# Optimization experiments

Measured on AMD Instinct MI355X. Metric: run time of the kernel, lower is better.

The kernel has to match this reference:

```python
import jax, jax.numpy as jnp
import numpy as np

NUM_LAYERS = 4
D_MODEL = 2
N_HALF = 32  # d_state // 2 complex modes
B, L = 512, 10000


def setup_inputs() -> dict:
    key = jax.random.key(0)
    ks = jax.random.split(key, 10)
    x = jax.random.normal(ks[0], (B, L, 3), dtype=jnp.float32)
    W1 = jax.random.normal(ks[1], (2, 3), dtype=jnp.float32) / np.float32(np.sqrt(3.0))
    b1 = jax.random.normal(ks[2], (2,), dtype=jnp.float32) * 0.1
    W2 = jax.random.normal(ks[3], (2, 2), dtype=jnp.float32) / np.float32(np.sqrt(2.0))
    b2 = jax.random.normal(ks[4], (2,), dtype=jnp.float32) * 0.1
    # S4D kernel params (stacked over layers)
    dt_min, dt_max = 1e-3, 1e-1
    log_dt = (jax.random.uniform(ks[5], (NUM_LAYERS, D_MODEL), dtype=jnp.float32)
              * np.float32(np.log(dt_max) - np.log(dt_min)) + np.float32(np.log(dt_min)))
    log_A_real = jnp.log(0.5 * jnp.ones((NUM_LAYERS, D_MODEL, N_HALF), dtype=jnp.float32))
    A_imag = (np.float32(np.pi) * jnp.arange(N_HALF, dtype=jnp.float32)
              * jnp.ones((NUM_LAYERS, D_MODEL, 1), dtype=jnp.float32))
    C = jax.random.normal(ks[6], (NUM_LAYERS, D_MODEL, N_HALF, 2), dtype=jnp.float32) * np.float32(0.5 ** 0.5)
    D = jax.random.normal(ks[7], (NUM_LAYERS, D_MODEL), dtype=jnp.float32)
    Wout = jax.random.normal(ks[8], (NUM_LAYERS, 2 * D_MODEL, D_MODEL), dtype=jnp.float32) / np.float32(np.sqrt(D_MODEL))
    bout = jax.random.normal(ks[9], (NUM_LAYERS, 2 * D_MODEL), dtype=jnp.float32) * 0.1
    return dict(x=x, W1=W1, b1=b1, W2=W2, b2=b2, log_dt=log_dt,
                log_A_real=log_A_real, A_imag=A_imag, C=C, D=D, Wout=Wout, bout=bout)


def _s4d_kernel(log_dt, log_A_real, A_imag, C, Lk):
    # log_dt: (H,), log_A_real/A_imag: (H,N), C: (H,N,2) -> kernel (H,Lk)
    dt = jnp.exp(log_dt)                              # (H,)
    Cc = C[..., 0] + 1j * C[..., 1]                   # (H,N) complex
    A = -jnp.exp(log_A_real) + 1j * A_imag            # (H,N)
    dtA = A * dt[:, None]                             # (H,N)
    K = dtA[:, :, None] * jnp.arange(Lk)              # (H,N,Lk)
    Cn = Cc * (jnp.exp(dtA) - 1.0) / A                # (H,N)
    return 2.0 * jnp.einsum('hn,hnl->hl', Cn, jnp.exp(K)).real


def reference(x, W1, b1, W2, b2, log_dt, log_A_real, A_imag, C, D, Wout, bout):
    Lseq = x.shape[1]
    h = x @ W1.T + b1                                 # (B,L,2)
    u = jnp.transpose(h, (0, 2, 1))                   # (B,H,L)
    for i in range(NUM_LAYERS):
        k = _s4d_kernel(log_dt[i], log_A_real[i], A_imag[i], C[i], Lseq)  # (H,L)
        kf = jnp.fft.rfft(k, n=2 * Lseq)              # (H,L+1)
        uf = jnp.fft.rfft(u, n=2 * Lseq)              # (B,H,L+1)
        y = jnp.fft.irfft(uf * kf, n=2 * Lseq)[..., :Lseq]  # linear conv via 2L FFT
        y = y + u * D[i][:, None]                     # skip connection
        y = jax.nn.gelu(y, approximate=False)
        y = jnp.einsum('oh,bhl->bol', Wout[i], y) + bout[i][None, :, None]  # Conv1d(H,2H,1)
        a, g = jnp.split(y, 2, axis=1)                # GLU over channel dim
        u = a * jax.nn.sigmoid(g)
    h = jnp.transpose(u, (0, 2, 1))                   # (B,L,2)
    return h @ W2.T + b2
```

## Files before the change

### kernel.cpp

```cpp
#include <hip/hip_runtime.h>
#include <hip/hip_bf16.h>
#include <math.h>

#define BB 512
#define LL 10000
#define HH 2
#define NN 32
#define NL 4
#define TT 64
#define CHK 157
#define CPAD 160
#define BL (BB*LL)

#define OFF_U0   0
#define OFF_U1   10240000
#define OFF_S0   20480000
#define OFF_S1   30769152
#define OFF_TAB  41058304

typedef _Float16 half8 __attribute__((ext_vector_type(8)));
typedef float f32x4 __attribute__((ext_vector_type(4)));

__global__ void setup_kernel(const float* __restrict__ log_dt,
                             const float* __restrict__ log_A_real,
                             const float* __restrict__ A_imag,
                             const float* __restrict__ Cin,
                             float* __restrict__ lam, float* __restrict__ lamT,
                             float* __restrict__ Cn, float* __restrict__ Kt,
                             float* __restrict__ P) {
    int ih = blockIdx.x;
    int tid = threadIdx.x;
    __shared__ float s_dtA[NN * 2];
    __shared__ float s_Cn[NN * 2];
    float dt = expf(log_dt[ih]);
    if (tid < NN) {
        int n = tid;
        float aRe = -expf(log_A_real[ih * NN + n]);
        float aIm = A_imag[ih * NN + n];
        float dRe = aRe * dt, dIm = aIm * dt;
        s_dtA[2 * n] = dRe; s_dtA[2 * n + 1] = dIm;
        float e = expf(dRe);
        float sn, cs; sincosf(dIm, &sn, &cs);
        float lRe = e * cs, lIm = e * sn;
        lam[ih * NN * 2 + 2 * n] = lRe;
        lam[ih * NN * 2 + 2 * n + 1] = lIm;
        float eT = expf((float)TT * dRe);
        float snT, csT; sincosf((float)TT * dIm, &snT, &csT);
        lamT[ih * NN * 2 + 2 * n] = eT * csT;
        lamT[ih * NN * 2 + 2 * n + 1] = eT * snT;
        float C0 = Cin[(ih * NN + n) * 2];
        float C1 = Cin[(ih * NN + n) * 2 + 1];
        float numRe = lRe - 1.0f, numIm = lIm;
        float den = aRe * aRe + aIm * aIm;
        float qRe = (numRe * aRe + numIm * aIm) / den;
        float qIm = (numIm * aRe - numRe * aIm) / den;
        float cnRe = C0 * qRe - C1 * qIm;
        float cnIm = C0 * qIm + C1 * qRe;
        Cn[ih * NN * 2 + 2 * n] = cnRe;
        Cn[ih * NN * 2 + 2 * n + 1] = cnIm;
        s_Cn[2 * n] = cnRe; s_Cn[2 * n + 1] = cnIm;
        for (int l = 0; l < TT; l++) {
            float p = (float)(l + 1);
            float ee = expf(p * dRe);
            float ss, cc; sincosf(p * dIm, &ss, &cc);
            P[(ih * NN + n) * TT * 2 + 2 * l]     = ee * cc;
            P[(ih * NN + n) * TT * 2 + 2 * l + 1] = ee * ss;
        }
    }
    __syncthreads();
    int d = tid;
    float acc = 0.0f;
    for (int n = 0; n < NN; n++) {
        float dRe = s_dtA[2 * n], dIm = s_dtA[2 * n + 1];
        float ee = expf((float)d * dRe);
        float ss, cc; sincosf((float)d * dIm, &ss, &cc);
        acc += s_Cn[2 * n] * (ee * cc) - s_Cn[2 * n + 1] * (ee * ss);
    }
    Kt[ih * TT + d] = 2.0f * acc;
}

__global__ void setup2_kernel(const float* __restrict__ Kt,
                              const float* __restrict__ P,
                              _Float16* __restrict__ AF,
                              _Float16* __restrict__ EF) {
    int ih = blockIdx.x;
    int lane = threadIdx.x;
    for (int kt = 0; kt < 4; kt++) {
        for (int lt = 0; lt < 4; lt++) {
            int l = lt * 16 + (lane & 15);
            int kbase = kt * 32 + (lane >> 4) * 8;
            for (int j = 0; j < 8; j++) {
                int k = kbase + j;
                float v;
                if (k < 64) {
                    int d = l - k;
                    v = (d >= 0) ? Kt[ih * TT + d] : 0.0f;
                } else {
                    int j2 = k - 64;
                    int n = j2 >> 1;
                    float pre = P[(ih * NN + n) * TT * 2 + 2 * l];
                    float pim = P[(ih * NN + n) * TT * 2 + 2 * l + 1];
                    v = (j2 & 1) ? (-2.0f * pim) : (2.0f * pre);
                }
                float hi = __uint_as_float(__float_as_uint(v) & 0xFFFFE000u);
                float lo = v - hi;
                size_t o0 = ((((size_t)ih * 2 + 0) * 4 + kt) * 4 + lt) * 512 + lane * 8 + j;
                size_t o1 = ((((size_t)ih * 2 + 1) * 4 + kt) * 4 + lt) * 512 + lane * 8 + j;
                AF[o0] = (_Float16)hi;
                AF[o1] = (_Float16)lo;
            }
        }
    }
    for (int kt = 0; kt < 2; kt++) {
        for (int lt = 0; lt < 4; lt++) {
            int row = lt * 16 + (lane & 15);
            int n = row >> 1, isIm = row & 1;
            int kbase = kt * 32 + (lane >> 4) * 8;
            for (int j = 0; j < 8; j++) {
                int k = kbase + j;
                int pw = 63 - k;
                float v;
                if (pw == 0) v = isIm ? 0.0f : 1.0f;
                else v = P[(ih * NN + n) * TT * 2 + 2 * (pw - 1) + isIm];
                float hi = __uint_as_float(__float_as_uint(v) & 0xFFFFE000u);
                float lo = v - hi;
                size_t o0 = ((((size_t)ih * 2 + 0) * 2 + kt) * 4 + lt) * 512 + lane * 8 + j;
                size_t o1 = ((((size_t)ih * 2 + 1) * 2 + kt) * 4 + lt) * 512 + lane * 8 + j;
                EF[o0] = (_Float16)hi;
                EF[o1] = (_Float16)lo;
            }
        }
    }
}

__global__ __launch_bounds__(256) void embed_kernel(const float* __restrict__ x,
                             const float* __restrict__ W1, const float* __restrict__ b1,
                             float* __restrict__ u) {
    int idx = blockIdx.x * blockDim.x + threadIdx.x;
    if (idx >= BL) return;
    int b = idx / LL, l = idx - b * LL;
    float x0 = x[idx * 3], x1 = x[idx * 3 + 1], x2 = x[idx * 3 + 2];
    float u0 = fmaf(W1[0], x0, fmaf(W1[1], x1, fmaf(W1[2], x2, b1[0])));
    float u1 = fmaf(W1[3], x0, fmaf(W1[4], x1, fmaf(W1[5], x2, b1[1])));
    u[(b * HH + 0) * LL + l] = u0;
    u[(b * HH + 1) * LL + l] = u1;
}

__device__ __forceinline__ void splitB(const f32x4& f0, const f32x4& f1,
                                       half8& Bh, half8& Bl) {
#pragma unroll
    for (int e = 0; e < 8; e++) {
        float v = (e < 4) ? f0[e] : f1[e - 4];
        float hi = __uint_as_float(__float_as_uint(v) & 0xFFFFE000u);
        Bh[e] = (_Float16)hi;
        Bl[e] = (_Float16)(v - hi);
    }
}

__global__ __launch_bounds__(256) void phaseA_mfma(const float* __restrict__ u,
                              const _Float16* __restrict__ EF,
                              float* __restrict__ stRaw) {
    const int wv = threadIdx.x >> 6;
    const int lane = threadIdx.x & 63;
    const int quad = lane >> 4;
    const int li = lane & 15;
    const int gw = blockIdx.x * 4 + wv;
    const int col = gw * 16 + li;
    const int b = col / CPAD;
    const int c = col - b * CPAD;
    const int cc = (c < CHK) ? c : (CHK - 1);
    const float* uB = u + (size_t)(b * HH) * LL + cc * TT;

    f32x4 eacc[4][2];
#pragma unroll
    for (int lt = 0; lt < 4; lt++)
#pragma unroll
        for (int ch = 0; ch < 2; ch++) eacc[lt][ch] = (f32x4){0.f, 0.f, 0.f, 0.f};

#pragma unroll
    for (int ch = 0; ch < 2; ch++) {
#pragma unroll
        for (int kt = 0; kt < 2; kt++) {
            const float* src = uB + ch * LL + kt * 32 + quad * 8;
            f32x4 f0 = *(const f32x4*)src;
            f32x4 f1 = *(const f32x4*)(src + 4);
            half8 Bh, Bl; splitB(f0, f1, Bh, Bl);
            const _Float16* efb = EF + (size_t)ch * 8192 + kt * 2048 + lane * 8;
#pragma unroll
            for (int lt = 0; lt < 4; lt++) {
                half8 Eh = *(const half8*)(efb + lt * 512);
                half8 El = *(const half8*)(efb + 4096 + lt * 512);
                eacc[lt][ch] = __builtin_amdgcn_mfma_f32_16x16x32_f16(Eh, Bh, eacc[lt][ch], 0, 0, 0);
                eacc[lt][ch] = __builtin_amdgcn_mfma_f32_16x16x32_f16(Eh, Bl, eacc[lt][ch], 0, 0, 0);
                eacc[lt][ch] = __builtin_amdgcn_mfma_f32_16x16x32_f16(El, Bh, eacc[lt][ch], 0, 0, 0);
            }
        }
    }
    if (c < CHK) {
        float* sp = stRaw + ((size_t)b * CHK + c) * 128;
#pragma unroll
        for (int ch = 0; ch < 2; ch++)
#pragma unroll
            for (int lt = 0; lt < 4; lt++)
                *(f32x4*)(sp + ch * 64 + lt * 16 + quad * 4) = eacc[lt][ch];
    }
}

__global__ __launch_bounds__(64) void phaseB_kernel(const float* __restrict__ lamT,
                              const float* __restrict__ CnT,
                              const float* __restrict__ stRaw,
                              float* __restrict__ stW, int layer) {
    int b = blockIdx.x;
    int lane = threadIdx.x;
    int h = lane >> 5, n = lane & 31;
    float lRe = lamT[(layer * HH + h) * NN * 2 + 2 * n];
    float lIm = lamT[(layer * HH + h) * NN * 2 + 2 * n + 1];
    float cRe = CnT[(layer * HH + h) * NN * 2 + 2 * n];
    float cIm = CnT[(layer * HH + h) * NN * 2 + 2 * n + 1];
    const float2* src = (const float2*)(stRaw + (size_t)b * CHK * 128) + lane;
    float2* dst = (float2*)(stW + (size_t)b * CHK * 128) + lane;
    float2 buf[8];
#pragma unroll
    for (int p = 0; p < 8; p++) buf[p] = src[(size_t)p * 64];
    float rRe = 0.f, rIm = 0.f;
    for (int co = 0; co < 20; co++) {
#pragma unroll
        for (int ci = 0; ci < 8; ci++) {
            int cx = co * 8 + ci;
            if (cx < CHK) {
                float2 v = buf[ci];
                if (cx + 8 < CHK) buf[ci] = src[(size_t)(cx + 8) * 64];
                float2 w;
                w.x = cRe * rRe - cIm * rIm;
                w.y = cRe * rIm + cIm * rRe;
                dst[(size_t)cx * 64] = w;
                float tRe = fmaf(lRe, rRe, fmaf(-lIm, rIm, v.x));
                float tIm = fmaf(lRe, rIm, fmaf(lIm, rRe, v.y));
                rRe = tRe; rIm = tIm;
            }
        }
    }
}

__global__ __launch_bounds__(256) void phaseC_mfma(
        const float* __restrict__ u, float* __restrict__ uNext,
        const _Float16* __restrict__ AF, const _Float16* __restrict__ EF,
        const float* __restrict__ stW, float* __restrict__ stRaw,
        const float* __restrict__ Dp, const float* __restrict__ Wout,
        const float* __restrict__ bout, int layer,
        const float* __restrict__ W2, const float* __restrict__ b2,
        float* __restrict__ out, int isLast) {
    const int wv = threadIdx.x >> 6;
    const int lane = threadIdx.x & 63;
    const int quad = lane >> 4;
    const int li = lane & 15;
    const int gw = blockIdx.x * 4 + wv;
    const int col = gw * 16 + li;
    const int b = col / CPAD;
    const int c = col - b * CPAD;
    const int cc = (c < CHK) ? c : (CHK - 1);
    const float* uB = u + (size_t)(b * HH) * LL + cc * TT;
    const float* wB = stW + ((size_t)b * CHK + cc) * 128;

    f32x4 acc[4][2];
#pragma unroll
    for (int lt = 0; lt < 4; lt++)
#pragma unroll
        for (int ch = 0; ch < 2; ch++) acc[lt][ch] = (f32x4){0.f, 0.f, 0.f, 0.f};

#pragma unroll
    for (int kt = 0; kt < 4; kt++) {
#pragma unroll
        for (int ch = 0; ch < 2; ch++) {
            const _Float16* afb = AF + (size_t)(layer * 2 + ch) * 16384 + kt * 2048 + lane * 8;
            const float* src = (kt < 2)
                ? (uB + ch * LL + kt * 32 + quad * 8)
                : (wB + ch * 64 + (kt - 2) * 32 + quad * 8);
            f32x4 f0 = *(const f32x4*)src;
            f32x4 f1 = *(const f32x4*)(src + 4);
            half8 Bh, Bl; splitB(f0, f1, Bh, Bl);
#pragma unroll
            for (int lt = 0; lt < 4; lt++) {
                half8 Ah = *(const half8*)(afb + lt * 512);
                half8 Al = *(const half8*)(afb + 8192 + lt * 512);
                acc[lt][ch] = __builtin_amdgcn_mfma_f32_16x16x32_f16(Ah, Bh, acc[lt][ch], 0, 0, 0);
                acc[lt][ch] = __builtin_amdgcn_mfma_f32_16x16x32_f16(Ah, Bl, acc[lt][ch], 0, 0, 0);
                acc[lt][ch] = __builtin_amdgcn_mfma_f32_16x16x32_f16(Al, Bh, acc[lt][ch], 0, 0, 0);
            }
        }
    }

    float D0 = Dp[layer * HH + 0], D1 = Dp[layer * HH + 1];
    const float* Wo = Wout + layer * 8;
    const float* bo = bout + layer * 4;
    bool cOK = (c < CHK);
    f32x4 r0f[4], r1f[4];
#pragma unroll
    for (int lt = 0; lt < 4; lt++) {
        int l = lt * 16 + quad * 4;
        f32x4 u0 = *(const f32x4*)(uB + l);
        f32x4 u1 = *(const f32x4*)(uB + LL + l);
        f32x4 r0, r1;
#pragma unroll
        for (int r = 0; r < 4; r++) {
            float a0 = fmaf(D0, u0[r], acc[lt][0][r]);
            float a1 = fmaf(D1, u1[r], acc[lt][1][r]);
            a0 = 0.5f * a0 * (1.0f + erff(a0 * 0.70710678118654752f));
            a1 = 0.5f * a1 * (1.0f + erff(a1 * 0.70710678118654752f));
            float z0 = fmaf(Wo[0], a0, fmaf(Wo[1], a1, bo[0]));
            float z1 = fmaf(Wo[2], a0, fmaf(Wo[3], a1, bo[1]));
            float z2 = fmaf(Wo[4], a0, fmaf(Wo[5], a1, bo[2]));
            float z3 = fmaf(Wo[6], a0, fmaf(Wo[7], a1, bo[3]));
            float g2 = 1.0f / (1.0f + expf(-z2));
            float g3 = 1.0f / (1.0f + expf(-z3));
            r0[r] = z0 * g2;
            r1[r] = z1 * g3;
        }
        r0f[lt] = r0; r1f[lt] = r1;
        bool ok = cOK && (c < CHK - 1 || lt == 0);
        if (!isLast) {
            if (ok) {
                float* p0 = uNext + (size_t)(b * HH) * LL + cc * TT + l;
                *(f32x4*)p0 = r0;
                *(f32x4*)(p0 + LL) = r1;
            }
        } else {
            if (ok) {
                float w20 = W2[0], w21 = W2[1], w22 = W2[2], w23 = W2[3];
                float b20 = b2[0], b21 = b2[1];
                float* op = out + ((size_t)b * LL + (size_t)cc * TT + l) * 2;
                f32x4 lo4, hi4;
                lo4[0] = fmaf(r0[0], w20, fmaf(r1[0], w21, b20));
                lo4[1] = fmaf(r0[0], w22, fmaf(r1[0], w23, b21));
                lo4[2] = fmaf(r0[1], w20, fmaf(r1[1], w21, b20));
                lo4[3] = fmaf(r0[1], w22, fmaf(r1[1], w23, b21));
                hi4[0] = fmaf(r0[2], w20, fmaf(r1[2], w21, b20));
                hi4[1] = fmaf(r0[2], w22, fmaf(r1[2], w23, b21));
                hi4[2] = fmaf(r0[3], w20, fmaf(r1[3], w21, b20));
                hi4[3] = fmaf(r0[3], w22, fmaf(r1[3], w23, b21));
                *(f32x4*)op = lo4;
                *(f32x4*)(op + 4) = hi4;
            }
        }
    }

    if (!isLast) {
        f32x4 rmA[4], rmB[4];
#pragma unroll
        for (int lt = 0; lt < 4; lt++) {
            bool z = (c == CHK - 1) && (lt > 0);
            rmA[lt] = z ? (f32x4){0.f, 0.f, 0.f, 0.f} : r0f[lt];
            rmB[lt] = z ? (f32x4){0.f, 0.f, 0.f, 0.f} : r1f[lt];
        }
        f32x4 eacc[4][2];
#pragma unroll
        for (int lt = 0; lt < 4; lt++)
#pragma unroll
            for (int ch = 0; ch < 2; ch++) eacc[lt][ch] = (f32x4){0.f, 0.f, 0.f, 0.f};

#pragma unroll
        for (int ch = 0; ch < 2; ch++) {
#pragma unroll
            for (int kt = 0; kt < 2; kt++) {
                float bv[8];
#pragma unroll
                for (int j = 0; j < 8; j++) {
                    int srcLane = ((quad & 1) * 2 + (j >> 2)) * 16 + li;
                    float x0 = ch ? rmB[kt * 2 + 0][j & 3] : rmA[kt * 2 + 0][j & 3];
                    float x1 = ch ? rmB[kt * 2 + 1][j & 3] : rmA[kt * 2 + 1][j & 3];
                    float a = __shfl(x0, srcLane, 64);
                    float bb = __shfl(x1, srcLane, 64);
                    bv[j] = (quad & 2) ? bb : a;
                }
                half8 Bh, Bl;
#pragma unroll
                for (int e = 0; e < 8; e++) {
                    float v = bv[e];
                    float hi = __uint_as_float(__float_as_uint(v) & 0xFFFFE000u);
                    Bh[e] = (_Float16)hi;
                    Bl[e] = (_Float16)(v - hi);
                }
                const _Float16* efb = EF + (size_t)layer * 16384 + (layer >= 0 ? 0 : 0)
                                      + (size_t)(ch + 1 - 1) * 0;
                efb = EF + ((size_t)(layer + 1) * 2 + ch) * 8192 + kt * 2048 + lane * 8;
#pragma unroll
                for (int lt = 0; lt < 4; lt++) {
                    half8 Eh = *(const half8*)(efb + lt * 512);
                    half8 El = *(const half8*)(efb + 4096 + lt * 512);
                    eacc[lt][ch] = __builtin_amdgcn_mfma_f32_16x16x32_f16(Eh, Bh, eacc[lt][ch], 0, 0, 0);
                    eacc[lt][ch] = __builtin_amdgcn_mfma_f32_16x16x32_f16(Eh, Bl, eacc[lt][ch], 0, 0, 0);
                    eacc[lt][ch] = __builtin_amdgcn_mfma_f32_16x16x32_f16(El, Bh, eacc[lt][ch], 0, 0, 0);
                }
            }
        }
        if (cOK) {
            float* sp = stRaw + ((size_t)b * CHK + c) * 128;
#pragma unroll
            for (int ch = 0; ch < 2; ch++)
#pragma unroll
                for (int lt = 0; lt < 4; lt++)
                    *(f32x4*)(sp + ch * 64 + lt * 16 + quad * 4) = eacc[lt][ch];
        }
    }
}

extern "C" void kernel_launch(void* const* d_in, const int* in_sizes, int n_in,
                              void* d_out, int out_size, void* d_ws, size_t ws_size,
                              hipStream_t stream) {
    const float* x         = (const float*)d_in[0];
    const float* W1        = (const float*)d_in[1];
    const float* b1        = (const float*)d_in[2];
    const float* W2        = (const float*)d_in[3];
    const float* b2        = (const float*)d_in[4];
    const float* log_dt    = (const float*)d_in[5];
    const float* log_A_real= (const float*)d_in[6];
    const float* A_imag    = (const float*)d_in[7];
    const float* Cin       = (const float*)d_in[8];
    const float* Dp        = (const float*)d_in[9];
    const float* Wout      = (const float*)d_in[10];
    const float* bout      = (const float*)d_in[11];
    float* out = (float*)d_out;
    float* ws = (float*)d_ws;

    float* U0   = ws + OFF_U0;
    float* U1   = ws + OFF_U1;
    float* S0   = ws + OFF_S0;
    float* S1   = ws + OFF_S1;
    float* lam  = ws + OFF_TAB;
    float* lamT = lam + 512;
    float* Cn   = lamT + 512;
    float* Kt   = Cn + 512;
    float* P    = Kt + 512;
    _Float16* AF = (_Float16*)(P + 32768);
    _Float16* EF = AF + 131072;

    setup_kernel<<<dim3(NL * HH), dim3(64), 0, stream>>>(log_dt, log_A_real, A_imag, Cin,
                                                         lam, lamT, Cn, Kt, P);
    setup2_kernel<<<dim3(NL * HH), dim3(64), 0, stream>>>(Kt, P, AF, EF);
    embed_kernel<<<dim3(BL / 256), dim3(256), 0, stream>>>(x, W1, b1, U0);
    phaseA_mfma<<<dim3(BB * CPAD / 64), dim3(256), 0, stream>>>(U0, EF, S0);

    float* cur = U0;
    float* nxt = U1;
    for (int i = 0; i < NL; i++) {
        phaseB_kernel<<<dim3(BB), dim3(64), 0, stream>>>(lamT, Cn, S0, S1, i);
        phaseC_mfma<<<dim3(BB * CPAD / 64), dim3(256), 0, stream>>>(cur, nxt, AF, EF, S1, S0,
                                                                    Dp, Wout, bout, i,
                                                                    W2, b2, out,
                                                                    (i == NL - 1) ? 1 : 0);
        float* tmp = cur; cur = nxt; nxt = tmp;
    }
}
```

Measured before the change: 438.8 us.

## Fuse all layers into one per-batch kernel keeping activations and states in LDS

Replaces the embed, phaseA, and per-layer phaseB/phaseC launches with a single kernel that has one 512-thread block per batch row. The sequence activations (2x10000 floats) and chunk states stay in shared memory across all four layers, using a padded stride and rotated indexing to reduce bank conflicts. This removes the repeated global round-trips of u and state buffers and the launch overhead. In exchange, about 200KB of LDS per block limits occupancy to one block per CU, and the serial chunk scan runs on a single wave while the other seven waves wait at a barrier.

Result: slower. 666.8 us (+52.0%).

```diff
diff --git a/kernel.cpp b/kernel.cpp
--- a/kernel.cpp
+++ b/kernel.cpp
@@ -9,14 +9,8 @@
 #define NL 4
 #define TT 64
 #define CHK 157
-#define CPAD 160
-#define BL (BB*LL)
-
-#define OFF_U0   0
-#define OFF_U1   10240000
-#define OFF_S0   20480000
-#define OFF_S1   30769152
-#define OFF_TAB  41058304
+#define SU_STRIDE 66
+#define SU_CH (CHK*SU_STRIDE)
 
 typedef _Float16 half8 __attribute__((ext_vector_type(8)));
 typedef float f32x4 __attribute__((ext_vector_type(4)));
@@ -133,19 +127,6 @@
     }
 }
 
-__global__ __launch_bounds__(256) void embed_kernel(const float* __restrict__ x,
-                             const float* __restrict__ W1, const float* __restrict__ b1,
-                             float* __restrict__ u) {
-    int idx = blockIdx.x * blockDim.x + threadIdx.x;
-    if (idx >= BL) return;
-    int b = idx / LL, l = idx - b * LL;
-    float x0 = x[idx * 3], x1 = x[idx * 3 + 1], x2 = x[idx * 3 + 2];
-    float u0 = fmaf(W1[0], x0, fmaf(W1[1], x1, fmaf(W1[2], x2, b1[0])));
-    float u1 = fmaf(W1[3], x0, fmaf(W1[4], x1, fmaf(W1[5], x2, b1[1])));
-    u[(b * HH + 0) * LL + l] = u0;
-    u[(b * HH + 1) * LL + l] = u1;
-}
-
 __device__ __forceinline__ void splitB(const f32x4& f0, const f32x4& f1,
                                        half8& Bh, half8& Bl) {
 #pragma unroll
@@ -157,250 +138,295 @@
     }
 }
 
-__global__ __launch_bounds__(256) void phaseA_mfma(const float* __restrict__ u,
-                              const _Float16* __restrict__ EF,
-                              float* __restrict__ stRaw) {
-    const int wv = threadIdx.x >> 6;
-    const int lane = threadIdx.x & 63;
-    const int quad = lane >> 4;
-    const int li = lane & 15;
-    const int gw = blockIdx.x * 4 + wv;
-    const int col = gw * 16 + li;
-    const int b = col / CPAD;
-    const int c = col - b * CPAD;
-    const int cc = (c < CHK) ? c : (CHK - 1);
-    const float* uB = u + (size_t)(b * HH) * LL + cc * TT;
-
+__device__ __forceinline__ void stateGemmStore(const half8* Bh, const half8* Bl,
+        const _Float16* __restrict__ EFl, float* s_st, int c, int lane) {
+    int quad = lane >> 4;
     f32x4 eacc[4][2];
 #pragma unroll
     for (int lt = 0; lt < 4; lt++)
 #pragma unroll
         for (int ch = 0; ch < 2; ch++) eacc[lt][ch] = (f32x4){0.f, 0.f, 0.f, 0.f};
-
-#pragma unroll
-    for (int ch = 0; ch < 2; ch++) {
+#pragma unroll
+    for (int ch = 0; ch < 2; ch++)
 #pragma unroll
         for (int kt = 0; kt < 2; kt++) {
-            const float* src = uB + ch * LL + kt * 32 + quad * 8;
-            f32x4 f0 = *(const f32x4*)src;
-            f32x4 f1 = *(const f32x4*)(src + 4);
-            half8 Bh, Bl; splitB(f0, f1, Bh, Bl);
-            const _Float16* efb = EF + (size_t)ch * 8192 + kt * 2048 + lane * 8;
+            const _Float16* efb = EFl + ch * 8192 + kt * 2048 + lane * 8;
+            half8 bh = Bh[ch * 2 + kt], bl = Bl[ch * 2 + kt];
 #pragma unroll
             for (int lt = 0; lt < 4; lt++) {
                 half8 Eh = *(const half8*)(efb + lt * 512);
                 half8 El = *(const half8*)(efb + 4096 + lt * 512);
-                eacc[lt][ch] = __builtin_amdgcn_mfma_f32_16x16x32_f16(Eh, Bh, eacc[lt][ch], 0, 0, 0);
-                eacc[lt][ch] = __builtin_amdgcn_mfma_f32_16x16x32_f16(Eh, Bl, eacc[lt][ch], 0, 0, 0);
-                eacc[lt][ch] = __builtin_amdgcn_mfma_f32_16x16x32_f16(El, Bh, eacc[lt][ch], 0, 0, 0);
-            }
-        }
-    }
+                eacc[lt][ch] = __builtin_amdgcn_mfma_f32_16x16x32_f16(Eh, bh, eacc[lt][ch], 0, 0, 0);
+                eacc[lt][ch] = __builtin_amdgcn_mfma_f32_16x16x32_f16(Eh, bl, eacc[lt][ch], 0, 0, 0);
+                eacc[lt][ch] = __builtin_amdgcn_mfma_f32_16x16x32_f16(El, bh, eacc[lt][ch], 0, 0, 0);
+            }
+        }
     if (c < CHK) {
-        float* sp = stRaw + ((size_t)b * CHK + c) * 128;
 #pragma unroll
         for (int ch = 0; ch < 2; ch++)
 #pragma unroll
-            for (int lt = 0; lt < 4; lt++)
-                *(f32x4*)(sp + ch * 64 + lt * 16 + quad * 4) = eacc[lt][ch];
-    }
-}
-
-__global__ __launch_bounds__(64) void phaseB_kernel(const float* __restrict__ lamT,
-                              const float* __restrict__ CnT,
-                              const float* __restrict__ stRaw,
-                              float* __restrict__ stW, int layer) {
-    int b = blockIdx.x;
-    int lane = threadIdx.x;
-    int h = lane >> 5, n = lane & 31;
-    float lRe = lamT[(layer * HH + h) * NN * 2 + 2 * n];
-    float lIm = lamT[(layer * HH + h) * NN * 2 + 2 * n + 1];
-    float cRe = CnT[(layer * HH + h) * NN * 2 + 2 * n];
-    float cIm = CnT[(layer * HH + h) * NN * 2 + 2 * n + 1];
-    const float2* src = (const float2*)(stRaw + (size_t)b * CHK * 128) + lane;
-    float2* dst = (float2*)(stW + (size_t)b * CHK * 128) + lane;
-    float2 buf[8];
-#pragma unroll
-    for (int p = 0; p < 8; p++) buf[p] = src[(size_t)p * 64];
-    float rRe = 0.f, rIm = 0.f;
-    for (int co = 0; co < 20; co++) {
-#pragma unroll
-        for (int ci = 0; ci < 8; ci++) {
-            int cx = co * 8 + ci;
-            if (cx < CHK) {
-                float2 v = buf[ci];
-                if (cx + 8 < CHK) buf[ci] = src[(size_t)(cx + 8) * 64];
-                float2 w;
-                w.x = cRe * rRe - cIm * rIm;
-                w.y = cRe * rIm + cIm * rRe;
-                dst[(size_t)cx * 64] = w;
-                float tRe = fmaf(lRe, rRe, fmaf(-lIm, rIm, v.x));
-                float tIm = fmaf(lRe, rIm, fmaf(lIm, rRe, v.y));
-                rRe = tRe; rIm = tIm;
-            }
-        }
-    }
-}
-
-__global__ __launch_bounds__(256) void phaseC_mfma(
-        const float* __restrict__ u, float* __restrict__ uNext,
+            for (int lt = 0; lt < 4; lt++) {
+                int idx = ch * 64 + lt * 16 + quad * 4;
+                int p0 = (idx + 2 * c) & 127;
+                int p1 = (idx + 2 + 2 * c) & 127;
+                *(float2*)(s_st + c * 128 + p0) = make_float2(eacc[lt][ch][0], eacc[lt][ch][1]);
+                *(float2*)(s_st + c * 128 + p1) = make_float2(eacc[lt][ch][2], eacc[lt][ch][3]);
+            }
+    }
+}
+
+__device__ __forceinline__ void loadUFrag(const float* s_u, int ch, int cc, int kt, int quad,
+                                          half8& bh, half8& bl) {
+    const float* p = s_u + ch * SU_CH + cc * SU_STRIDE + kt * 32 + quad * 8;
+    float2 a = *(const float2*)p;
+    float2 b = *(const float2*)(p + 2);
+    float2 c = *(const float2*)(p + 4);
+    float2 d = *(const float2*)(p + 6);
+    f32x4 f0 = {a.x, a.y, b.x, b.y};
+    f32x4 f1 = {c.x, c.y, d.x, d.y};
+    splitB(f0, f1, bh, bl);
+}
+
+__global__ __launch_bounds__(512) void mega_kernel(
+        const float* __restrict__ x,
+        const float* __restrict__ W1, const float* __restrict__ b1,
+        const float* __restrict__ lamT, const float* __restrict__ CnT,
         const _Float16* __restrict__ AF, const _Float16* __restrict__ EF,
-        const float* __restrict__ stW, float* __restrict__ stRaw,
         const float* __restrict__ Dp, const float* __restrict__ Wout,
-        const float* __restrict__ bout, int layer,
+        const float* __restrict__ bout,
         const float* __restrict__ W2, const float* __restrict__ b2,
-        float* __restrict__ out, int isLast) {
-    const int wv = threadIdx.x >> 6;
-    const int lane = threadIdx.x & 63;
+        float* __restrict__ out) {
+    __shared__ float s_u[2 * SU_CH];
+    __shared__ float s_st[CHK * 128];
+    const int tid = threadIdx.x;
+    const int w8 = tid >> 6;
+    const int lane = tid & 63;
     const int quad = lane >> 4;
     const int li = lane & 15;
-    const int gw = blockIdx.x * 4 + wv;
-    const int col = gw * 16 + li;
-    const int b = col / CPAD;
-    const int c = col - b * CPAD;
-    const int cc = (c < CHK) ? c : (CHK - 1);
-    const float* uB = u + (size_t)(b * HH) * LL + cc * TT;
-    const float* wB = stW + ((size_t)b * CHK + cc) * 128;
-
-    f32x4 acc[4][2];
-#pragma unroll
-    for (int lt = 0; lt < 4; lt++)
-#pragma unroll
-        for (int ch = 0; ch < 2; ch++) acc[lt][ch] = (f32x4){0.f, 0.f, 0.f, 0.f};
-
-#pragma unroll
-    for (int kt = 0; kt < 4; kt++) {
-#pragma unroll
-        for (int ch = 0; ch < 2; ch++) {
-            const _Float16* afb = AF + (size_t)(layer * 2 + ch) * 16384 + kt * 2048 + lane * 8;
-            const float* src = (kt < 2)
-                ? (uB + ch * LL + kt * 32 + quad * 8)
-                : (wB + ch * 64 + (kt - 2) * 32 + quad * 8);
-            f32x4 f0 = *(const f32x4*)src;
-            f32x4 f1 = *(const f32x4*)(src + 4);
-            half8 Bh, Bl; splitB(f0, f1, Bh, Bl);
+    const int b = blockIdx.x;
+
+    {
+        const float w10 = W1[0], w11 = W1[1], w12 = W1[2];
+        const float w13 = W1[3], w14 = W1[4], w15 = W1[5];
+        const float bb0 = b1[0], bb1 = b1[1];
+        for (int g = tid; g < 2500; g += 512) {
+            int l = 4 * g;
+            const float4* xp = (const float4*)(x + ((size_t)b * LL + l) * 3);
+            float4 xa = xp[0], xb = xp[1], xc = xp[2];
+            float t0[3] = {xa.x, xa.y, xa.z}, t1[3] = {xa.w, xb.x, xb.y};
+            float t2[3] = {xb.z, xb.w, xc.x}, t3[3] = {xc.y, xc.z, xc.w};
+            int c = l >> 6, t = l & 63;
+            float u00 = fmaf(w10, t0[0], fmaf(w11, t0[1], fmaf(w12, t0[2], bb0)));
+            float u01 = fmaf(w10, t1[0], fmaf(w11, t1[1], fmaf(w12, t1[2], bb0)));
+            float u02 = fmaf(w10, t2[0], fmaf(w11, t2[1], fmaf(w12, t2[2], bb0)));
+            float u03 = fmaf(w10, t3[0], fmaf(w11, t3[1], fmaf(w12, t3[2], bb0)));
+            float u10 = fmaf(w13, t0[0], fmaf(w14, t0[1], fmaf(w15, t0[2], bb1)));
+            float u11 = fmaf(w13, t1[0], fmaf(w14, t1[1], fmaf(w15, t1[2], bb1)));
+            float u12 = fmaf(w13, t2[0], fmaf(w14, t2[1], fmaf(w15, t2[2], bb1)));
+            float u13 = fmaf(w13, t3[0], fmaf(w14, t3[1], fmaf(w15, t3[2], bb1)));
+            float* p0 = s_u + c * SU_STRIDE + t;
+            float* p1 = p0 + SU_CH;
+            *(float2*)p0 = make_float2(u00, u01);
+            *(float2*)(p0 + 2) = make_float2(u02, u03);
+            *(float2*)p1 = make_float2(u10, u11);
+            *(float2*)(p1 + 2) = make_float2(u12, u13);
+        }
+        if (tid < 96) {
+            int ch = tid / 48, t = 16 + (tid % 48);
+            s_u[ch * SU_CH + 156 * SU_STRIDE + t] = 0.0f;
+        }
+    }
+    __syncthreads();
+
+    for (int T = w8; T < 10; T += 8) {
+        int c = T * 16 + li;
+        int cc = (c < CHK) ? c : (CHK - 1);
+        half8 Bh[4], Bl[4];
+#pragma unroll
+        for (int ch = 0; ch < 2; ch++)
+#pragma unroll
+            for (int kt = 0; kt < 2; kt++)
+                loadUFrag(s_u, ch, cc, kt, quad, Bh[ch * 2 + kt], Bl[ch * 2 + kt]);
+        stateGemmStore(Bh, Bl, EF, s_st, c, lane);
+    }
+    __syncthreads();
+
+    for (int i = 0; i < NL; i++) {
+        const bool isLast = (i == NL - 1);
+
+        if (w8 == 0) {
+            int h = lane >> 5, n = lane & 31;
+            float lRe = lamT[(i * HH + h) * NN * 2 + 2 * n];
+            float lIm = lamT[(i * HH + h) * NN * 2 + 2 * n + 1];
+            float cRe = CnT[(i * HH + h) * NN * 2 + 2 * n];
+            float cIm = CnT[(i * HH + h) * NN * 2 + 2 * n + 1];
+            int idx0 = h * 64 + 2 * n;
+            float rRe = 0.f, rIm = 0.f;
+            float2 v = *(const float2*)(s_st + (idx0 & 127));
+            for (int c = 0; c < CHK; c++) {
+                float2 vc = v;
+                if (c + 1 < CHK) {
+                    int pn = (idx0 + 2 * (c + 1)) & 127;
+                    v = *(const float2*)(s_st + (c + 1) * 128 + pn);
+                }
+                float wRe = cRe * rRe - cIm * rIm;
+                float wIm = cRe * rIm + cIm * rRe;
+                int pw = (idx0 + 2 * c) & 127;
+                *(float2*)(s_st + c * 128 + pw) = make_float2(wRe, wIm);
+                float tRe = fmaf(lRe, rRe, fmaf(-lIm, rIm, vc.x));
+                float tIm = fmaf(lRe, rIm, fmaf(lIm, rRe, vc.y));
+                rRe = tRe; rIm = tIm;
+            }
+        }
+        __syncthreads();
+
+        float D0 = Dp[i * HH + 0], D1 = Dp[i * HH + 1];
+        const float* Wo = Wout + i * 8;
+        const float* bo = bout + i * 4;
+        float w20 = W2[0], w21 = W2[1], w22 = W2[2], w23 = W2[3];
+        float b20 = b2[0], b21 = b2[1];
+
+        for (int T = w8; T < 10; T += 8) {
+            int c = T * 16 + li;
+            int cc = (c < CHK) ? c : (CHK - 1);
+            bool cOK = (c < CHK);
+
+            half8 uh[2][2], ul2[2][2], wh[2][2], wl[2][2];
+#pragma unroll
+            for (int ch = 0; ch < 2; ch++)
+#pragma unroll
+                for (int kt = 0; kt < 2; kt++)
+                    loadUFrag(s_u, ch, cc, kt, quad, uh[ch][kt], ul2[ch][kt]);
+#pragma unroll
+            for (int ch = 0; ch < 2; ch++)
+#pragma unroll
+                for (int k2 = 0; k2 < 2; k2++) {
+                    int idx2 = ch * 64 + k2 * 32 + quad * 8;
+                    float tmp[8];
+#pragma unroll
+                    for (int jj = 0; jj < 4; jj++) {
+                        int pp = (idx2 + 2 * jj + 2 * cc) & 127;
+                        float2 vv = *(const float2*)(s_st + cc * 128 + pp);
+                        tmp[2 * jj] = vv.x; tmp[2 * jj + 1] = vv.y;
+                    }
+                    f32x4 f0 = {tmp[0], tmp[1], tmp[2], tmp[3]};
+                    f32x4 f1 = {tmp[4], tmp[5], tmp[6], tmp[7]};
+                    splitB(f0, f1, wh[ch][k2], wl[ch][k2]);
+                }
+
+            f32x4 acc[4][2];
+#pragma unroll
+            for (int lt = 0; lt < 4; lt++)
+#pragma unroll
+                for (int ch = 0; ch < 2; ch++) acc[lt][ch] = (f32x4){0.f, 0.f, 0.f, 0.f};
+#pragma unroll
+            for (int kt = 0; kt < 4; kt++)
+#pragma unroll
+                for (int ch = 0; ch < 2; ch++) {
+                    const _Float16* afb = AF + (size_t)(i * 2 + ch) * 16384 + kt * 2048 + lane * 8;
+                    half8 Bh = (kt < 2) ? uh[ch][kt] : wh[ch][kt - 2];
+                    half8 Bl = (kt < 2) ? ul2[ch][kt] : wl[ch][kt - 2];
+#pragma unroll
+                    for (int lt = 0; lt < 4; lt++) {
+                        half8 Ah = *(const half8*)(afb + lt * 512);
+                        half8 Al = *(const half8*)(afb + 8192 + lt * 512);
+                        acc[lt][ch] = __builtin_amdgcn_mfma_f32_16x16x32_f16(Ah, Bh, acc[lt][ch], 0, 0, 0);
+                        acc[lt][ch] = __builtin_amdgcn_mfma_f32_16x16x32_f16(Ah, Bl, acc[lt][ch], 0, 0, 0);
+                        acc[lt][ch] = __builtin_amdgcn_mfma_f32_16x16x32_f16(Al, Bh, acc[lt][ch], 0, 0, 0);
+                    }
+                }
+
+            f32x4 r0f[4], r1f[4];
 #pragma unroll
             for (int lt = 0; lt < 4; lt++) {
-                half8 Ah = *(const half8*)(afb + lt * 512);
-                half8 Al = *(const half8*)(afb + 8192 + lt * 512);
-                acc[lt][ch] = __builtin_amdgcn_mfma_f32_16x16x32_f16(Ah, Bh, acc[lt][ch], 0, 0, 0);
-                acc[lt][ch] = __builtin_amdgcn_mfma_f32_16x16x32_f16(Ah, Bl, acc[lt][ch], 0, 0, 0);
-                acc[lt][ch] = __builtin_amdgcn_mfma_f32_16x16x32_f16(Al, Bh, acc[lt][ch], 0, 0, 0);
-            }
-        }
-    }
-
-    float D0 = Dp[layer * HH + 0], D1 = Dp[layer * HH + 1];
-    const float* Wo = Wout + layer * 8;
-    const float* bo = bout + layer * 4;
-    bool cOK = (c < CHK);
-    f32x4 r0f[4], r1f[4];
-#pragma unroll
-    for (int lt = 0; lt < 4; lt++) {
-        int l = lt * 16 + quad * 4;
-        f32x4 u0 = *(const f32x4*)(uB + l);
-        f32x4 u1 = *(const f32x4*)(uB + LL + l);
-        f32x4 r0, r1;
-#pragma unroll
-        for (int r = 0; r < 4; r++) {
-            float a0 = fmaf(D0, u0[r], acc[lt][0][r]);
-            float a1 = fmaf(D1, u1[r], acc[lt][1][r]);
-            a0 = 0.5f * a0 * (1.0f + erff(a0 * 0.70710678118654752f));
-            a1 = 0.5f * a1 * (1.0f + erff(a1 * 0.70710678118654752f));
-            float z0 = fmaf(Wo[0], a0, fmaf(Wo[1], a1, bo[0]));
-            float z1 = fmaf(Wo[2], a0, fmaf(Wo[3], a1, bo[1]));
-            float z2 = fmaf(Wo[4], a0, fmaf(Wo[5], a1, bo[2]));
-            float z3 = fmaf(Wo[6], a0, fmaf(Wo[7], a1, bo[3]));
-            float g2 = 1.0f / (1.0f + expf(-z2));
-            float g3 = 1.0f / (1.0f + expf(-z3));
-            r0[r] = z0 * g2;
-            r1[r] = z1 * g3;
-        }
-        r0f[lt] = r0; r1f[lt] = r1;
-        bool ok = cOK && (c < CHK - 1 || lt == 0);
-        if (!isLast) {
-            if (ok) {
-                float* p0 = uNext + (size_t)(b * HH) * LL + cc * TT + l;
-                *(f32x4*)p0 = r0;
-                *(f32x4*)(p0 + LL) = r1;
-            }
-        } else {
-            if (ok) {
-                float w20 = W2[0], w21 = W2[1], w22 = W2[2], w23 = W2[3];
-                float b20 = b2[0], b21 = b2[1];
-                float* op = out + ((size_t)b * LL + (size_t)cc * TT + l) * 2;
-                f32x4 lo4, hi4;
-                lo4[0] = fmaf(r0[0], w20, fmaf(r1[0], w21, b20));
-                lo4[1] = fmaf(r0[0], w22, fmaf(r1[0], w23, b21));
-                lo4[2] = fmaf(r0[1], w20, fmaf(r1[1], w21, b20));
-                lo4[3] = fmaf(r0[1], w22, fmaf(r1[1], w23, b21));
-                hi4[0] = fmaf(r0[2], w20, fmaf(r1[2], w21, b20));
-                hi4[1] = fmaf(r0[2], w22, fmaf(r1[2], w23, b21));
-                hi4[2] = fmaf(r0[3], w20, fmaf(r1[3], w21, b20));
-                hi4[3] = fmaf(r0[3], w22, fmaf(r1[3], w23, b21));
-                *(f32x4*)op = lo4;
-                *(f32x4*)(op + 4) = hi4;
-            }
-        }
-    }
-
-    if (!isLast) {
-        f32x4 rmA[4], rmB[4];
-#pragma unroll
-        for (int lt = 0; lt < 4; lt++) {
-            bool z = (c == CHK - 1) && (lt > 0);
-            rmA[lt] = z ? (f32x4){0.f, 0.f, 0.f, 0.f} : r0f[lt];
-            rmB[lt] = z ? (f32x4){0.f, 0.f, 0.f, 0.f} : r1f[lt];
-        }
-        f32x4 eacc[4][2];
-#pragma unroll
-        for (int lt = 0; lt < 4; lt++)
-#pragma unroll
-            for (int ch = 0; ch < 2; ch++) eacc[lt][ch] = (f32x4){0.f, 0.f, 0.f, 0.f};
-
-#pragma unroll
-        for (int ch = 0; ch < 2; ch++) {
-#pragma unroll
-            for (int kt = 0; kt < 2; kt++) {
-                float bv[8];
-#pragma unroll
-                for (int j = 0; j < 8; j++) {
-                    int srcLane = ((quad & 1) * 2 + (j >> 2)) * 16 + li;
-                    float x0 = ch ? rmB[kt * 2 + 0][j & 3] : rmA[kt * 2 + 0][j & 3];
-                    float x1 = ch ? rmB[kt * 2 + 1][j & 3] : rmA[kt * 2 + 1][j & 3];
-                    float a = __shfl(x0, srcLane, 64);
-                    float bb = __shfl(x1, srcLane, 64);
-                    bv[j] = (quad & 2) ? bb : a;
-                }
-                half8 Bh, Bl;
-#pragma unroll
-                for (int e = 0; e < 8; e++) {
-                    float v = bv[e];
-                    float hi = __uint_as_float(__float_as_uint(v) & 0xFFFFE000u);
-                    Bh[e] = (_Float16)hi;
-                    Bl[e] = (_Float16)(v - hi);
-                }
-                const _Float16* efb = EF + (size_t)layer * 16384 + (layer >= 0 ? 0 : 0)
-                                      + (size_t)(ch + 1 - 1) * 0;
-                efb = EF + ((size_t)(layer + 1) * 2 + ch) * 8192 + kt * 2048 + lane * 8;
+                int l = lt * 16 + quad * 4;
+                const float* pu0 = s_u + cc * SU_STRIDE + l;
+                const float* pu1 = pu0 + SU_CH;
+                float2 ua = *(const float2*)pu0, ub = *(const float2*)(pu0 + 2);
+                float2 uc = *(const float2*)pu1, ud = *(const float2*)(pu1 + 2);
+                f32x4 u0 = {ua.x, ua.y, ub.x, ub.y};
+                f32x4 u1 = {uc.x, uc.y, ud.x, ud.y};
+                f32x4 r0, r1;
+#pragma unroll
+                for (int r = 0; r < 4; r++) {
+                    float a0 = fmaf(D0, u0[r], acc[lt][0][r]);
+                    float a1 = fmaf(D1, u1[r], acc[lt][1][r]);
+                    a0 = 0.5f * a0 * (1.0f + erff(a0 * 0.70710678118654752f));
+                    a1 = 0.5f * a1 * (1.0f + erff(a1 * 0.70710678118654752f));
+                    float z0 = fmaf(Wo[0], a0, fmaf(Wo[1], a1, bo[0]));
+                    float z1 = fmaf(Wo[2], a0, fmaf(Wo[3], a1, bo[1]));
+                    float z2 = fmaf(Wo[4], a0, fmaf(Wo[5], a1, bo[2]));
+                    float z3 = fmaf(Wo[6], a0, fmaf(Wo[7], a1, bo[3]));
+                    float g2 = 1.0f / (1.0f + expf(-z2));
+                    float g3 = 1.0f / (1.0f + expf(-z3));
+                    r0[r] = z0 * g2;
+                    r1[r] = z1 * g3;
+                }
+                r0f[lt] = r0; r1f[lt] = r1;
+                bool ok = cOK && (c < CHK - 1 || lt == 0);
+                if (!isLast) {
+                    if (ok) {
+                        float* pd0 = s_u + cc * SU_STRIDE + l;
+                        float* pd1 = pd0 + SU_CH;
+                        *(float2*)pd0 = make_float2(r0[0], r0[1]);
+                        *(float2*)(pd0 + 2) = make_float2(r0[2], r0[3]);
+                        *(float2*)pd1 = make_float2(r1[0], r1[1]);
+                        *(float2*)(pd1 + 2) = make_float2(r1[2], r1[3]);
+                    }
+                } else if (ok) {
+                    float* op = out + ((size_t)b * LL + (size_t)cc * TT + l) * 2;
+                    f32x4 lo4, hi4;
+                    lo4[0] = fmaf(r0[0], w20, fmaf(r1[0], w21, b20));
+                    lo4[1] = fmaf(r0[0], w22, fmaf(r1[0], w23, b21));
+                    lo4[2] = fmaf(r0[1], w20, fmaf(r1[1], w21, b20));
+                    lo4[3] = fmaf(r0[1], w22, fmaf(r1[1], w23, b21));
+                    hi4[0] = fmaf(r0[2], w20, fmaf(r1[2], w21, b20));
+                    hi4[1] = fmaf(r0[2], w22, fmaf(r1[2], w23, b21));
+                    hi4[2] = fmaf(r0[3], w20, fmaf(r1[3], w21, b20));
+                    hi4[3] = fmaf(r0[3], w22, fmaf(r1[3], w23, b21));
+                    *(f32x4*)op = lo4;
+                    *(f32x4*)(op + 4) = hi4;
+                }
+            }
+
+            if (!isLast) {
+                f32x4 rmA[4], rmB[4];
 #pragma unroll
                 for (int lt = 0; lt < 4; lt++) {
-                    half8 Eh = *(const half8*)(efb + lt * 512);
-                    half8 El = *(const half8*)(efb + 4096 + lt * 512);
-                    eacc[lt][ch] = __builtin_amdgcn_mfma_f32_16x16x32_f16(Eh, Bh, eacc[lt][ch], 0, 0, 0);
-                    eacc[lt][ch] = __builtin_amdgcn_mfma_f32_16x16x32_f16(Eh, Bl, eacc[lt][ch], 0, 0, 0);
-                    eacc[lt][ch] = __builtin_amdgcn_mfma_f32_16x16x32_f16(El, Bh, eacc[lt][ch], 0, 0, 0);
-                }
-            }
-        }
-        if (cOK) {
-            float* sp = stRaw + ((size_t)b * CHK + c) * 128;
-#pragma unroll
-            for (int ch = 0; ch < 2; ch++)
-#pragma unroll
-                for (int lt = 0; lt < 4; lt++)
-                    *(f32x4*)(sp + ch * 64 + lt * 16 + quad * 4) = eacc[lt][ch];
-        }
+                    bool z = (c == CHK - 1) && (lt > 0);
+                    rmA[lt] = z ? (f32x4){0.f, 0.f, 0.f, 0.f} : r0f[lt];
+                    rmB[lt] = z ? (f32x4){0.f, 0.f, 0.f, 0.f} : r1f[lt];
+                }
+                half8 sbH[4], sbL[4];
+#pragma unroll
+                for (int ch = 0; ch < 2; ch++)
+#pragma unroll
+                    for (int kt = 0; kt < 2; kt++) {
+                        float bv[8];
+#pragma unroll
+                        for (int j = 0; j < 8; j++) {
+                            int srcLane = ((quad & 1) * 2 + (j >> 2)) * 16 + li;
+                            float x0 = ch ? rmB[kt * 2 + 0][j & 3] : rmA[kt * 2 + 0][j & 3];
+                            float x1 = ch ? rmB[kt * 2 + 1][j & 3] : rmA[kt * 2 + 1][j & 3];
+                            float a = __shfl(x0, srcLane, 64);
+                            float bb = __shfl(x1, srcLane, 64);
+                            bv[j] = (quad & 2) ? bb : a;
+                        }
+                        half8 Bh, Bl;
+#pragma unroll
+                        for (int e = 0; e < 8; e++) {
+                            float v = bv[e];
+                            float hi = __uint_as_float(__float_as_uint(v) & 0xFFFFE000u);
+                            Bh[e] = (_Float16)hi;
+                            Bl[e] = (_Float16)(v - hi);
+                        }
+                        sbH[ch * 2 + kt] = Bh;
+                        sbL[ch * 2 + kt] = Bl;
+                    }
+                stateGemmStore(sbH, sbL, EF + (size_t)(i + 1) * 16384, s_st, c, lane);
+            }
+        }
+        __syncthreads();
     }
 }
 
@@ -422,11 +448,7 @@
     float* out = (float*)d_out;
     float* ws = (float*)d_ws;
 
-    float* U0   = ws + OFF_U0;
-    float* U1   = ws + OFF_U1;
-    float* S0   = ws + OFF_S0;
-    float* S1   = ws + OFF_S1;
-    float* lam  = ws + OFF_TAB;
+    float* lam  = ws;
     float* lamT = lam + 512;
     float* Cn   = lamT + 512;
     float* Kt   = Cn + 512;
@@ -437,17 +459,6 @@
     setup_kernel<<<dim3(NL * HH), dim3(64), 0, stream>>>(log_dt, log_A_real, A_imag, Cin,
                                                          lam, lamT, Cn, Kt, P);
     setup2_kernel<<<dim3(NL * HH), dim3(64), 0, stream>>>(Kt, P, AF, EF);
-    embed_kernel<<<dim3(BL / 256), dim3(256), 0, stream>>>(x, W1, b1, U0);
-    phaseA_mfma<<<dim3(BB * CPAD / 64), dim3(256), 0, stream>>>(U0, EF, S0);
-
-    float* cur = U0;
-    float* nxt = U1;
-    for (int i = 0; i < NL; i++) {
-        phaseB_kernel<<<dim3(BB), dim3(64), 0, stream>>>(lamT, Cn, S0, S1, i);
-        phaseC_mfma<<<dim3(BB * CPAD / 64), dim3(256), 0, stream>>>(cur, nxt, AF, EF, S1, S0,
-                                                                    Dp, Wout, bout, i,
-                                                                    W2, b2, out,
-                                                                    (i == NL - 1) ? 1 : 0);
-        float* tmp = cur; cur = nxt; nxt = tmp;
-    }
-}
+    mega_kernel<<<dim3(BB), dim3(512), 0, stream>>>(x, W1, b1, lamT, Cn, AF, EF,
+                                                    Dp, Wout, bout, W2, b2, out);
+}
```
